# Optimization experiments

Hardware: AMD Instinct MI355X
Metric: run time of the kernel (lower is better)

Reference implementation:

```python
import jax, jax.numpy as jnp
import numpy as np

N = 100000      # nodes
E = 1600000     # edges
F_IN = 128      # input feature dim (x_s)
H = 64          # neuron
CF = 16         # attention_num_feature
G = 256         # graphs in batch


def setup_inputs() -> dict:
    key = jax.random.key(0)
    ks = jax.random.split(key, 20)
    w = lambda k, s: (jax.random.normal(k, s, jnp.float32) * 0.1)
    return {
        "x": jax.random.normal(ks[0], (N, F_IN), jnp.float32),
        "edge_index": jax.random.randint(ks[1], (2, E), 0, N, dtype=jnp.int64),
        "batch": jnp.sort(jax.random.randint(ks[2], (N,), 0, G, dtype=jnp.int64)),
        "closeness": jax.random.normal(ks[3], (N, CF), jnp.float32),
        "W1l": w(ks[4], (F_IN, H)), "b1l": jnp.zeros((H,), jnp.float32), "W1r": w(ks[5], (F_IN, H)),
        "W2l": w(ks[6], (H, H)),   "b2l": jnp.zeros((H,), jnp.float32), "W2r": w(ks[7], (H, H)),
        "W3l": w(ks[8], (H, H)),   "b3l": jnp.zeros((H,), jnp.float32), "W3r": w(ks[9], (H, H)),
        "Wc": w(ks[10], (CF, 1)),  "bc": jnp.zeros((1,), jnp.float32),
        "Wa1": w(ks[11], (H, 16)), "ba1": jnp.zeros((16,), jnp.float32),
        "Wa2": w(ks[12], (16, 1)), "ba2": jnp.zeros((1,), jnp.float32),
    }


def _sage_conv_max(x, src, dst, Wl, bl, Wr):
    # PyG SAGEConv(aggr='max'): lin_l(max_j x_j) + lin_r(x_i)
    msg = x[src]                                            # [E, F]
    agg = jax.ops.segment_max(msg, dst, num_segments=N)     # [N, F]
    agg = jnp.where(jnp.isfinite(agg), agg, 0.0)            # empty neighborhoods -> 0
    return agg @ Wl + bl + x @ Wr


def reference(x, edge_index, batch, closeness,
              W1l, b1l, W1r, W2l, b2l, W2r, W3l, b3l, W3r,
              Wc, bc, Wa1, ba1, Wa2, ba2):
    src, dst = edge_index[0], edge_index[1]
    h = jax.nn.relu(_sage_conv_max(x, src, dst, W1l, b1l, W1r))
    h = jax.nn.relu(_sage_conv_max(h, src, dst, W2l, b2l, W2r))
    h = jax.nn.relu(_sage_conv_max(h, src, dst, W3l, b3l, W3r))   # [N, H]

    # per-graph softmax attention (self_max aggregator), fused via segment ops
    c = closeness @ Wc + bc                                  # [N, 1]
    cmax = jax.ops.segment_max(c, batch, num_segments=G)     # [G, 1]
    e = jnp.exp(c - cmax[batch])                             # [N, 1]
    denom = jax.ops.segment_sum(e, batch, num_segments=G)    # [G, 1]
    p = e / denom[batch]                                     # softmax within each graph
    counts = jax.ops.segment_sum(jnp.ones((x.shape[0],), jnp.float32), batch, num_segments=G)
    p = p * counts[batch][:, None]                           # * curr_size

    pooled = jax.ops.segment_max(p * h, batch, num_segments=G)   # [G, H]
    pooled = jnp.where(jnp.isfinite(pooled), pooled, 0.0)
    a = jax.nn.relu(pooled @ Wa1 + ba1)
    return a @ Wa2 + ba2                                     # [G, 1]
```

## Files before the change

### kernel.cpp

```cpp
#include <hip/hip_runtime.h>
#include <math.h>

typedef unsigned int uint32;
typedef __attribute__((ext_vector_type(8))) short short8;
typedef __attribute__((ext_vector_type(4))) float f32x4;

#define BSH 7
#define NBMAX 800
#define CHUNK 4096


__device__ __forceinline__ unsigned fkey(float f) {
  unsigned u = __float_as_uint(f);
  return (u & 0x80000000u) ? ~u : (u | 0x80000000u);
}
__device__ __forceinline__ float funkey(unsigned k) {
  unsigned u = (k & 0x80000000u) ? (k ^ 0x80000000u) : ~k;
  return __uint_as_float(u);
}
__device__ __forceinline__ unsigned short f2bf(float f) {
  unsigned u = __float_as_uint(f);
  unsigned r = (u + 0x7FFFu + ((u >> 16) & 1u)) >> 16;
  return (unsigned short)r;
}
__device__ __forceinline__ float bf2f(unsigned short s) {
  return __uint_as_float(((unsigned)s) << 16);
}
__device__ __forceinline__ float blo(uint32 u) { return __uint_as_float(u << 16); }
__device__ __forceinline__ float bhi(uint32 u) { return __uint_as_float(u & 0xFFFF0000u); }
__device__ __forceinline__ uint32 cvtpk(float lo, float hi) {
  uint32 r;
  asm("v_cvt_pk_bf16_f32 %0, %1, %2" : "=v"(r) : "v"(lo), "v"(hi));
  return r;
}
__device__ __forceinline__ f32x4 mfma16(short8 a, short8 b, f32x4 c) {
  return __builtin_amdgcn_mfma_f32_16x16x32_bf16(a, b, c, 0, 0, 0);
}


__global__ void init_kernel(int* __restrict__ cnt, unsigned* __restrict__ pooledU,
                            unsigned* __restrict__ cmaxU, float* __restrict__ denom,
                            int* __restrict__ gcnt, int n, int gh, int g) {
  int i = blockIdx.x * blockDim.x + threadIdx.x;
  if (i < n) cnt[i] = 0;
  if (i < gh) pooledU[i] = 0x80000000u;
  if (i < g) { cmaxU[i] = 0u; denom[i] = 0.f; gcnt[i] = 0; }
}


__global__ void cvt_bf16_kernel(const float* __restrict__ in, unsigned short* __restrict__ out,
                                int n4) {
  int i = blockIdx.x * blockDim.x + threadIdx.x;
  if (i < n4) {
    float4 v = ((const float4*)in)[i];
    ushort4 o;
    o.x = f2bf(v.x);
    o.y = f2bf(v.y);
    o.z = f2bf(v.z);
    o.w = f2bf(v.w);
    ((ushort4*)out)[i] = o;
  }
}


__global__ void pack_bfrag_kernel(const float* __restrict__ W1l, const float* __restrict__ W1r,
                                  const float* __restrict__ W2l, const float* __restrict__ W2r,
                                  const float* __restrict__ W3l, const float* __restrict__ W3r,
                                  uint32* __restrict__ out) {
  int i = blockIdx.x * blockDim.x + threadIdx.x;
  if (i >= 32768) return;
  int set = i >> 14;
  int r = i & 16383;
  int g = r >> 8;
  int lane = (r >> 2) & 63;
  int p = r & 3;
  const float *Wl, *Wr;
  int F, nt, ks;
  if (g < 32) {
    F = 128; Wl = W1l; Wr = W1r; nt = g >> 3; ks = g & 7;
  } else if (g < 48) {
    F = 64; Wl = W2l; Wr = W2r; int q = g - 32; nt = q >> 2; ks = q & 3;
  } else {
    F = 64; Wl = W3l; Wr = W3r; int q = g - 48; nt = q >> 2; ks = q & 3;
  }
  int col = nt * 16 + (lane & 15);
  int k0 = ks * 32 + ((lane >> 4) << 3) + 2 * p;
  float w0 = (k0 < F) ? Wl[k0 * 64 + col] : Wr[(k0 - F) * 64 + col];
  int k1 = k0 + 1;
  float w1 = (k1 < F) ? Wl[k1 * 64 + col] : Wr[(k1 - F) * 64 + col];
  if (set) {
    w0 -= bf2f(f2bf(w0));
    w1 -= bf2f(f2bf(w1));
  }
  out[i] = ((uint32)f2bf(w1) << 16) | (uint32)f2bf(w0);
}


__global__ void hist_kernel(const int* __restrict__ dst, int* __restrict__ hist,
                            int E, int NB, int NC) {
  __shared__ int lcnt[NBMAX];
  int t = threadIdx.x, c = blockIdx.x;
  for (int i = t; i < NB; i += 256) lcnt[i] = 0;
  __syncthreads();
  int e0 = c * CHUNK, e1 = min(e0 + CHUNK, E);
  for (int e = e0 + t; e < e1; e += 256) atomicAdd(&lcnt[dst[e] >> BSH], 1);
  __syncthreads();
  for (int i = t; i < NB; i += 256) hist[(size_t)i * NC + c] = lcnt[i];
}

__global__ void rowscan_kernel(int* __restrict__ hist, int* __restrict__ bsum, int NB, int NC) {
  int wv = blockIdx.x * 4 + (threadIdx.x >> 6);
  int lane = threadIdx.x & 63;
  if (wv >= NB) return;
  int* row = hist + (size_t)wv * NC;
  int run = 0;
  for (int c = 0; c < NC; c += 64) {
    int idx = c + lane;
    int v = (idx < NC) ? row[idx] : 0;
    int incl = v;
#pragma unroll
    for (int off = 1; off < 64; off <<= 1) {
      int tt = __shfl_up(incl, off);
      if (lane >= off) incl += tt;
    }
    int tot = __shfl(incl, 63);
    if (idx < NC) row[idx] = run + incl - v;
    run += tot;
  }
  if (lane == 0) bsum[wv] = run;
}

__global__ void binscan_kernel(const int* __restrict__ bsum, int* __restrict__ bbase, int NB) {
  int lane = threadIdx.x;
  int run = 0;
  for (int c = 0; c < NB; c += 64) {
    int idx = c + lane;
    int v = (idx < NB) ? bsum[idx] : 0;
    int incl = v;
#pragma unroll
    for (int off = 1; off < 64; off <<= 1) {
      int tt = __shfl_up(incl, off);
      if (lane >= off) incl += tt;
    }
    if (idx < NB) bbase[idx] = run + incl - v;
    run += __shfl(incl, 63);
  }
  if (lane == 0) bbase[NB] = run;
}

__global__ void bfill_kernel(const int* __restrict__ src, const int* __restrict__ dst,
                             const int* __restrict__ hist, const int* __restrict__ bbase,
                             uint32* __restrict__ bbuf, int E, int NB, int NC) {
  __shared__ int lcur[NBMAX];
  int t = threadIdx.x, c = blockIdx.x;
  for (int i = t; i < NB; i += 256) lcur[i] = bbase[i] + hist[(size_t)i * NC + c];
  __syncthreads();
  int e0 = c * CHUNK, e1 = min(e0 + CHUNK, E);
  for (int e = e0 + t; e < e1; e += 256) {
    int d = dst[e], s = src[e];
    int b = d >> BSH;
    int pos = atomicAdd(&lcur[b], 1);
    bbuf[pos] = ((uint32)s << BSH) | (uint32)(d & ((1 << BSH) - 1));
  }
}

__global__ void place_kernel(const int* __restrict__ bbase, const uint32* __restrict__ bbuf,
                             int* __restrict__ cnt, int* __restrict__ csr, int N) {
  __shared__ int lcnt[1 << BSH];
  int b = blockIdx.x, t = threadIdx.x;
  for (int i = t; i < (1 << BSH); i += 256) lcnt[i] = 0;
  __syncthreads();
  int s0 = bbase[b], s1 = bbase[b + 1];
  for (int i = s0 + t; i < s1; i += 256) {
    uint32 rec = bbuf[i];
    int dl = rec & ((1 << BSH) - 1);
    int s = (int)(rec >> BSH);
    int pos = atomicAdd(&lcnt[dl], 1);
    if (pos < 64) csr[(((b << BSH) + dl) << 6) + pos] = s;
  }
  __syncthreads();
  int base = b << BSH;
  for (int i = t; i < (1 << BSH); i += 256) {
    int d = base + i;
    if (d < N) cnt[d] = min(lcnt[i], 64);
  }
}


template <int F, bool OUT_F32>
__global__ void __launch_bounds__(256, 2) sage_layer(
    const unsigned short* __restrict__ xg,
    const int* __restrict__ cnt, const int* __restrict__ csr,
    const short8* __restrict__ BfHi, const short8* __restrict__ BfLo, int loff,
    const float* __restrict__ bl, float* __restrict__ outf,
    unsigned short* __restrict__ outb, int nn) {
  constexpr int NPW = 8;
  constexpr int PAD = F + 4;
  constexpr int KS = F / 16;
  const int lane = threadIdx.x & 63;
  const int wid = threadIdx.x >> 6;
  const int c = lane & 31;
  const int h = lane >> 5;
  const int blk = blockIdx.x * 32;
  __shared__ uint32 Abuf[32][PAD];

  for (int j = 0; j < NPW; ++j) {
    int nl = wid * NPW + j;
    int n = blk + nl;
    if constexpr (F == 128) {
      float m0 = 0.f, m1 = 0.f, m2 = 0.f, m3 = 0.f;
      uint32 sv = 0u;
      if (n < nn) {
        sv = *(const uint32*)(xg + (size_t)n * F + 2 * lane);
        int dg = cnt[n];
        if (dg > 64) dg = 64;
        int k0 = n << 6, k1 = k0 + dg;
        if (k1 > k0) {
          m0 = -INFINITY; m1 = -INFINITY; m2 = -INFINITY; m3 = -INFINITY;
          int k = k0;
          for (; k + 8 <= k1; k += 8) {
            int i0 = csr[k + h], i1 = csr[k + 2 + h];
            int i2 = csr[k + 4 + h], i3 = csr[k + 6 + h];
            uint2 a = *(const uint2*)(xg + (size_t)i0 * F + 4 * c);
            uint2 b = *(const uint2*)(xg + (size_t)i1 * F + 4 * c);
            uint2 d = *(const uint2*)(xg + (size_t)i2 * F + 4 * c);
            uint2 e = *(const uint2*)(xg + (size_t)i3 * F + 4 * c);
            m0 = fmaxf(m0, fmaxf(fmaxf(blo(a.x), blo(b.x)), fmaxf(blo(d.x), blo(e.x))));
            m1 = fmaxf(m1, fmaxf(fmaxf(bhi(a.x), bhi(b.x)), fmaxf(bhi(d.x), bhi(e.x))));
            m2 = fmaxf(m2, fmaxf(fmaxf(blo(a.y), blo(b.y)), fmaxf(blo(d.y), blo(e.y))));
            m3 = fmaxf(m3, fmaxf(fmaxf(bhi(a.y), bhi(b.y)), fmaxf(bhi(d.y), bhi(e.y))));
          }
          for (; k + 2 <= k1; k += 2) {
            int i0 = csr[k + h];
            uint2 a = *(const uint2*)(xg + (size_t)i0 * F + 4 * c);
            m0 = fmaxf(m0, blo(a.x));
            m1 = fmaxf(m1, bhi(a.x));
            m2 = fmaxf(m2, blo(a.y));
            m3 = fmaxf(m3, bhi(a.y));
          }
          if (k < k1) {
            int i0 = csr[k];
            uint2 a = *(const uint2*)(xg + (size_t)i0 * F + 4 * c);
            m0 = fmaxf(m0, blo(a.x));
            m1 = fmaxf(m1, bhi(a.x));
            m2 = fmaxf(m2, blo(a.y));
            m3 = fmaxf(m3, bhi(a.y));
          }
          m0 = fmaxf(m0, __shfl_xor(m0, 32));
          m1 = fmaxf(m1, __shfl_xor(m1, 32));
          m2 = fmaxf(m2, __shfl_xor(m2, 32));
          m3 = fmaxf(m3, __shfl_xor(m3, 32));
        }
      }
      if (h == 0) {
        uint2 mm;
        mm.x = cvtpk(m0, m1);
        mm.y = cvtpk(m2, m3);
        *(uint2*)&Abuf[nl][2 * c] = mm;
      }
      Abuf[nl][64 + lane] = sv;
    } else {
      float m0 = 0.f, m1 = 0.f;
      uint32 sv = 0u;
      if (n < nn) {
        if (h == 0) sv = *(const uint32*)(xg + (size_t)n * F + 2 * c);
        int dg = cnt[n];
        if (dg > 64) dg = 64;
        int k0 = n << 6, k1 = k0 + dg;
        if (k1 > k0) {
          m0 = -INFINITY; m1 = -INFINITY;
          int k = k0;
          for (; k + 8 <= k1; k += 8) {
            int i0 = csr[k + h], i1 = csr[k + 2 + h];
            int i2 = csr[k + 4 + h], i3 = csr[k + 6 + h];
            uint32 a = *(const uint32*)(xg + (size_t)i0 * F + 2 * c);
            uint32 b = *(const uint32*)(xg + (size_t)i1 * F + 2 * c);
            uint32 d = *(const uint32*)(xg + (size_t)i2 * F + 2 * c);
            uint32 e = *(const uint32*)(xg + (size_t)i3 * F + 2 * c);
            m0 = fmaxf(m0, fmaxf(fmaxf(blo(a), blo(b)), fmaxf(blo(d), blo(e))));
            m1 = fmaxf(m1, fmaxf(fmaxf(bhi(a), bhi(b)), fmaxf(bhi(d), bhi(e))));
          }
          for (; k + 2 <= k1; k += 2) {
            int i0 = csr[k + h];
            uint32 a = *(const uint32*)(xg + (size_t)i0 * F + 2 * c);
            m0 = fmaxf(m0, blo(a));
            m1 = fmaxf(m1, bhi(a));
          }
          if (k < k1) {
            int i0 = csr[k];
            uint32 a = *(const uint32*)(xg + (size_t)i0 * F + 2 * c);
            m0 = fmaxf(m0, blo(a));
            m1 = fmaxf(m1, bhi(a));
          }
          m0 = fmaxf(m0, __shfl_xor(m0, 32));
          m1 = fmaxf(m1, __shfl_xor(m1, 32));
        }
      }
      if (h == 0) {
        Abuf[nl][c] = cvtpk(m0, m1);
        Abuf[nl][32 + c] = sv;
      }
    }
  }
  __syncthreads();

  const int l15 = lane & 15, lk = lane >> 4;
  const int mt = wid & 1;
  const int ntb = (wid >> 1) << 1;
  const int arow = mt * 16 + l15;
  float bb0 = bl[ntb * 16 + l15], bb1 = bl[ntb * 16 + 16 + l15];
  f32x4 acc0 = {bb0, bb0, bb0, bb0};
  f32x4 acc1 = {bb1, bb1, bb1, bb1};
  const int gb0 = (loff + (ntb + 0) * KS) * 64 + lane;
  const int gb1 = (loff + (ntb + 1) * KS) * 64 + lane;
#pragma unroll 2
  for (int ks = 0; ks < KS; ++ks) {
    short8 a = *(const short8*)&Abuf[arow][ks * 16 + lk * 4];
    short8 bh0 = BfHi[gb0 + ks * 64];
    short8 bl0 = BfLo[gb0 + ks * 64];
    short8 bh1 = BfHi[gb1 + ks * 64];
    short8 bl1 = BfLo[gb1 + ks * 64];
    acc0 = mfma16(a, bh0, acc0);
    acc0 = mfma16(a, bl0, acc0);
    acc1 = mfma16(a, bh1, acc1);
    acc1 = mfma16(a, bl1, acc1);
  }
#pragma unroll
  for (int j = 0; j < 4; ++j) {
    int node = blk + mt * 16 + lk * 4 + j;
    if (node < nn) {
      float r0 = fmaxf(acc0[j], 0.f);
      float r1 = fmaxf(acc1[j], 0.f);
      if constexpr (OUT_F32) {
        outf[(size_t)node * 64 + ntb * 16 + l15] = r0;
        outf[(size_t)node * 64 + ntb * 16 + 16 + l15] = r1;
      } else {
        outb[(size_t)node * 64 + ntb * 16 + l15] = f2bf(r0);
        outb[(size_t)node * 64 + ntb * 16 + 16 + l15] = f2bf(r1);
      }
    }
  }
}


__global__ void cscore_kernel(const float* __restrict__ clo, const float* __restrict__ Wc,
                              const float* __restrict__ bc, const int* __restrict__ bat,
                              float* __restrict__ cbuf, unsigned* __restrict__ cmaxU,
                              int* __restrict__ gcnt, int n) {
  int i = blockIdx.x * blockDim.x + threadIdx.x;
  int lane = threadIdx.x & 63;
  float cv = -INFINITY;
  int g = -1;
  if (i < n) {
    const float4* row = (const float4*)(clo + (size_t)i * 16);
    float4 r0 = row[0], r1 = row[1], r2 = row[2], r3 = row[3];
    cv = bc[0];
    cv += r0.x * Wc[0] + r0.y * Wc[1] + r0.z * Wc[2] + r0.w * Wc[3];
    cv += r1.x * Wc[4] + r1.y * Wc[5] + r1.z * Wc[6] + r1.w * Wc[7];
    cv += r2.x * Wc[8] + r2.y * Wc[9] + r2.z * Wc[10] + r2.w * Wc[11];
    cv += r3.x * Wc[12] + r3.y * Wc[13] + r3.z * Wc[14] + r3.w * Wc[15];
    cbuf[i] = cv;
    g = bat[i];
  }
  int g0 = __shfl(g, 0), g63 = __shfl(g, 63);
  if (g0 >= 0 && g0 == g63) {
    float m = cv;
#pragma unroll
    for (int off = 32; off; off >>= 1) m = fmaxf(m, __shfl_down(m, off));
    if (lane == 0) {
      atomicMax(&cmaxU[g0], fkey(m));
      atomicAdd(&gcnt[g0], 64);
    }
  } else if (g >= 0) {
    atomicMax(&cmaxU[g], fkey(cv));
    atomicAdd(&gcnt[g], 1);
  }
}

__global__ void esum_kernel(const float* __restrict__ cbuf, const int* __restrict__ bat,
                            const unsigned* __restrict__ cmaxU, float* __restrict__ ebuf,
                            float* __restrict__ denom, int n) {
  int i = blockIdx.x * blockDim.x + threadIdx.x;
  int lane = threadIdx.x & 63;
  float ev = 0.f;
  int g = -1;
  if (i < n) {
    g = bat[i];
    float cm = funkey(cmaxU[g]);
    ev = expf(cbuf[i] - cm);
    ebuf[i] = ev;
  }
  int g0 = __shfl(g, 0), g63 = __shfl(g, 63);
  if (g0 >= 0 && g0 == g63) {
    float s = ev;
#pragma unroll
    for (int off = 32; off; off >>= 1) s += __shfl_down(s, off);
    if (lane == 0) atomicAdd(&denom[g0], s);
  } else if (g >= 0) {
    atomicAdd(&denom[g], ev);
  }
}

__global__ void pool_kernel(const float* __restrict__ ebuf, const float* __restrict__ denom,
                            const int* __restrict__ gcnt, const int* __restrict__ bat,
                            const float* __restrict__ h3, unsigned* __restrict__ pooledU,
                            int n) {
  const int CH = 64;
  int wave = (blockIdx.x * blockDim.x + threadIdx.x) >> 6;
  int lane = threadIdx.x & 63;
  int nb = wave * CH;
  if (nb >= n) return;
  int ne = min(nb + CH, n);
  int curg = bat[nb];
  float factor = (float)gcnt[curg] / denom[curg];
  float lmax = -INFINITY;
  for (int nd = nb; nd < ne; ++nd) {
    int g = bat[nd];
    if (g != curg) {
      atomicMax(&pooledU[(size_t)curg * 64 + lane], fkey(lmax));
      curg = g;
      factor = (float)gcnt[g] / denom[g];
      lmax = -INFINITY;
    }
    float v = ebuf[nd] * factor * h3[(size_t)nd * 64 + lane];
    lmax = fmaxf(lmax, v);
  }
  atomicMax(&pooledU[(size_t)curg * 64 + lane], fkey(lmax));
}

__global__ void final_kernel(const unsigned* __restrict__ pooledU, const float* __restrict__ Wa1,
                             const float* __restrict__ ba1, const float* __restrict__ Wa2,
                             const float* __restrict__ ba2, float* __restrict__ out, int G) {
  int g = blockIdx.x;
  int lane = threadIdx.x;
  float v = funkey(pooledU[(size_t)g * 64 + lane]);
  if (!isfinite(v)) v = 0.f;
  float outv = 0.f;
#pragma unroll
  for (int j = 0; j < 16; ++j) {
    float psum = v * Wa1[lane * 16 + j];
#pragma unroll
    for (int off = 32; off; off >>= 1) psum += __shfl_down(psum, off);
    if (lane == 0) outv += fmaxf(psum + ba1[j], 0.f) * Wa2[j];
  }
  if (lane == 0) out[g] = outv + ba2[0];
}


static inline size_t alignup(size_t x) { return (x + 255) & ~(size_t)255; }

extern "C" void kernel_launch(void* const* d_in, const int* in_sizes, int n_in,
                              void* d_out, int out_size, void* d_ws, size_t ws_size,
                              hipStream_t stream) {
  const float* x = (const float*)d_in[0];
  const int* ei = (const int*)d_in[1];
  const int* bat = (const int*)d_in[2];
  const float* clo = (const float*)d_in[3];
  const float* W1l = (const float*)d_in[4];
  const float* b1l = (const float*)d_in[5];
  const float* W1r = (const float*)d_in[6];
  const float* W2l = (const float*)d_in[7];
  const float* b2l = (const float*)d_in[8];
  const float* W2r = (const float*)d_in[9];
  const float* W3l = (const float*)d_in[10];
  const float* b3l = (const float*)d_in[11];
  const float* W3r = (const float*)d_in[12];
  const float* Wc = (const float*)d_in[13];
  const float* bc = (const float*)d_in[14];
  const float* Wa1 = (const float*)d_in[15];
  const float* ba1 = (const float*)d_in[16];
  const float* Wa2 = (const float*)d_in[17];
  const float* ba2 = (const float*)d_in[18];
  float* out = (float*)d_out;

  const int N = in_sizes[2];
  const int E = in_sizes[1] / 2;
  const int G = out_size;
  const int FIN = in_sizes[0] / N;

  char* p = (char*)d_ws;
  auto carve = [&](size_t bytes) {
    char* r = p;
    p += alignup(bytes);
    return r;
  };
  const int NB = (N + (1 << BSH) - 1) >> BSH;
  const int NC = (E + CHUNK - 1) / CHUNK;
  int* cnt = (int*)carve((size_t)N * 4);
  int* csr = (int*)carve((size_t)N * 64 * 4);
  unsigned short* xb = (unsigned short*)carve((size_t)N * FIN * 2);
  unsigned short* hb1 = (unsigned short*)carve((size_t)N * 64 * 2);
  unsigned short* hb2 = (unsigned short*)carve((size_t)N * 64 * 2);
  float* cbuf = (float*)carve((size_t)N * 4);
  float* ebuf = (float*)carve((size_t)N * 4);
  unsigned* cmaxU = (unsigned*)carve((size_t)G * 4);
  float* denom = (float*)carve((size_t)G * 4);
  int* gcnt = (int*)carve((size_t)G * 4);
  unsigned* pooledU = (unsigned*)carve((size_t)G * 64 * 4);
  uint32* Bfrag = (uint32*)carve((size_t)32768 * 4);
  int* hist = (int*)carve((size_t)NB * NC * 4);
  int* bsum = (int*)carve((size_t)NB * 4);
  int* bbase = (int*)carve((size_t)(NB + 1) * 4);
  uint32* bbuf = (uint32*)carve((size_t)E * 4);
  float* h3 = (float*)xb;

  const short8* BfHi = (const short8*)Bfrag;
  const short8* BfLo = (const short8*)(Bfrag + 16384);

  const int* srcv = ei;
  const int* dstv = ei + E;

  int nb = (N + 255) / 256;
  hipLaunchKernelGGL(init_kernel, dim3(nb), dim3(256), 0, stream, cnt, pooledU, cmaxU, denom,
                     gcnt, N, G * 64, G);
  int ncvt = (N * FIN) / 4;
  hipLaunchKernelGGL(cvt_bf16_kernel, dim3((ncvt + 255) / 256), dim3(256), 0, stream, x, xb,
                     ncvt);
  hipLaunchKernelGGL(pack_bfrag_kernel, dim3(128), dim3(256), 0, stream, W1l, W1r, W2l, W2r,
                     W3l, W3r, Bfrag);
  hipLaunchKernelGGL(hist_kernel, dim3(NC), dim3(256), 0, stream, dstv, hist, E, NB, NC);
  hipLaunchKernelGGL(rowscan_kernel, dim3((NB + 3) / 4), dim3(256), 0, stream, hist, bsum, NB,
                     NC);
  hipLaunchKernelGGL(binscan_kernel, dim3(1), dim3(64), 0, stream, bsum, bbase, NB);
  hipLaunchKernelGGL(bfill_kernel, dim3(NC), dim3(256), 0, stream, srcv, dstv, hist, bbase,
                     bbuf, E, NB, NC);
  hipLaunchKernelGGL(place_kernel, dim3(NB), dim3(256), 0, stream, bbase, bbuf, cnt, csr, N);

  int nblocks32 = (N + 31) / 32;
  hipLaunchKernelGGL((sage_layer<128, false>), dim3(nblocks32), dim3(256), 0, stream, xb, cnt,
                     csr, BfHi, BfLo, 0, b1l, (float*)nullptr, hb1, N);
  hipLaunchKernelGGL((sage_layer<64, false>), dim3(nblocks32), dim3(256), 0, stream, hb1, cnt,
                     csr, BfHi, BfLo, 32, b2l, (float*)nullptr, hb2, N);
  hipLaunchKernelGGL((sage_layer<64, true>), dim3(nblocks32), dim3(256), 0, stream, hb2, cnt,
                     csr, BfHi, BfLo, 48, b3l, h3, (unsigned short*)nullptr, N);

  hipLaunchKernelGGL(cscore_kernel, dim3(nb), dim3(256), 0, stream, clo, Wc, bc, bat, cbuf,
                     cmaxU, gcnt, N);
  hipLaunchKernelGGL(esum_kernel, dim3(nb), dim3(256), 0, stream, cbuf, bat, cmaxU, ebuf, denom,
                     N);
  int pw = (N + 63) / 64;
  int pb = (pw + 3) / 4;
  hipLaunchKernelGGL(pool_kernel, dim3(pb), dim3(256), 0, stream, ebuf, denom, gcnt, bat, h3,
                     pooledU, N);
  hipLaunchKernelGGL(final_kernel, dim3(G), dim3(64), 0, stream, pooledU, Wa1, ba1, Wa2, ba2,
                     out, G);
}
```

Measured before the change: 491.3 us.

## Use order-preserving bf16 keys with packed u16 max for neighbor aggregation

Layer 1 input is stored as order-preserving 16-bit keys, so the neighbor max becomes v_pk_max_u16 on packed pairs with no unpacking to fp32, and results are un-keyed once per node. Layers 2 and 3 take non-negative post-ReLU bf16 values, whose raw bit patterns already order correctly, so they use the same packed unsigned max. The gather loop is unrolled to 16 edges per step for more loads in flight. The cnt zeroing is also dropped from init, which assumes place_kernel writes every cnt entry; negative zero in layers 2-3 and the empty-neighborhood zero both depend on these orderings holding.

```diff
diff --git a/kernel.cpp b/kernel.cpp
--- a/kernel.cpp
+++ b/kernel.cpp
@@ -26,38 +26,40 @@
 __device__ __forceinline__ float bf2f(unsigned short s) {
   return __uint_as_float(((unsigned)s) << 16);
 }
-__device__ __forceinline__ float blo(uint32 u) { return __uint_as_float(u << 16); }
-__device__ __forceinline__ float bhi(uint32 u) { return __uint_as_float(u & 0xFFFF0000u); }
-__device__ __forceinline__ uint32 cvtpk(float lo, float hi) {
-  uint32 r;
-  asm("v_cvt_pk_bf16_f32 %0, %1, %2" : "=v"(r) : "v"(lo), "v"(hi));
-  return r;
+__device__ __forceinline__ uint32 pkmaxu(uint32 a, uint32 b) {
+  uint32 d;
+  asm("v_pk_max_u16 %0, %1, %2" : "=v"(d) : "v"(a), "v"(b));
+  return d;
+}
+__device__ __forceinline__ uint32 unkey2(uint32 m) {
+  uint32 t = (m >> 15) & 0x00010001u;
+  uint32 mask = (t * 0x7FFFu) ^ 0xFFFFFFFFu;
+  return m ^ mask;
 }
 __device__ __forceinline__ f32x4 mfma16(short8 a, short8 b, f32x4 c) {
   return __builtin_amdgcn_mfma_f32_16x16x32_bf16(a, b, c, 0, 0, 0);
 }
 
 
-__global__ void init_kernel(int* __restrict__ cnt, unsigned* __restrict__ pooledU,
-                            unsigned* __restrict__ cmaxU, float* __restrict__ denom,
-                            int* __restrict__ gcnt, int n, int gh, int g) {
+__global__ void init_kernel(unsigned* __restrict__ pooledU, unsigned* __restrict__ cmaxU,
+                            float* __restrict__ denom, int* __restrict__ gcnt, int gh, int g) {
   int i = blockIdx.x * blockDim.x + threadIdx.x;
-  if (i < n) cnt[i] = 0;
   if (i < gh) pooledU[i] = 0x80000000u;
   if (i < g) { cmaxU[i] = 0u; denom[i] = 0.f; gcnt[i] = 0; }
 }
 
 
-__global__ void cvt_bf16_kernel(const float* __restrict__ in, unsigned short* __restrict__ out,
-                                int n4) {
+__global__ void cvt_key_kernel(const float* __restrict__ in, unsigned short* __restrict__ out,
+                               int n4) {
   int i = blockIdx.x * blockDim.x + threadIdx.x;
   if (i < n4) {
     float4 v = ((const float4*)in)[i];
     ushort4 o;
-    o.x = f2bf(v.x);
-    o.y = f2bf(v.y);
-    o.z = f2bf(v.z);
-    o.w = f2bf(v.w);
+    unsigned short b;
+    b = f2bf(v.x); o.x = (b & 0x8000u) ? (unsigned short)~b : (unsigned short)(b | 0x8000u);
+    b = f2bf(v.y); o.y = (b & 0x8000u) ? (unsigned short)~b : (unsigned short)(b | 0x8000u);
+    b = f2bf(v.z); o.z = (b & 0x8000u) ? (unsigned short)~b : (unsigned short)(b | 0x8000u);
+    b = f2bf(v.w); o.w = (b & 0x8000u) ? (unsigned short)~b : (unsigned short)(b | 0x8000u);
     ((ushort4*)out)[i] = o;
   }
 }
@@ -197,6 +199,7 @@
   constexpr int NPW = 8;
   constexpr int PAD = F + 4;
   constexpr int KS = F / 16;
+  constexpr bool KEYED = (F == 128);
   const int lane = threadIdx.x & 63;
   const int wid = threadIdx.x >> 6;
   const int c = lane & 31;
@@ -208,96 +211,82 @@
     int nl = wid * NPW + j;
     int n = blk + nl;
     if constexpr (F == 128) {
-      float m0 = 0.f, m1 = 0.f, m2 = 0.f, m3 = 0.f;
-      uint32 sv = 0u;
+      uint32 m01 = 0u, m23 = 0u, sv = 0u;
       if (n < nn) {
-        sv = *(const uint32*)(xg + (size_t)n * F + 2 * lane);
+        sv = *(const uint32*)(xg + ((size_t)n << 7) + 2 * lane);
         int dg = cnt[n];
         if (dg > 64) dg = 64;
         int k0 = n << 6, k1 = k0 + dg;
         if (k1 > k0) {
-          m0 = -INFINITY; m1 = -INFINITY; m2 = -INFINITY; m3 = -INFINITY;
           int k = k0;
-          for (; k + 8 <= k1; k += 8) {
-            int i0 = csr[k + h], i1 = csr[k + 2 + h];
-            int i2 = csr[k + 4 + h], i3 = csr[k + 6 + h];
-            uint2 a = *(const uint2*)(xg + (size_t)i0 * F + 4 * c);
-            uint2 b = *(const uint2*)(xg + (size_t)i1 * F + 4 * c);
-            uint2 d = *(const uint2*)(xg + (size_t)i2 * F + 4 * c);
-            uint2 e = *(const uint2*)(xg + (size_t)i3 * F + 4 * c);
-            m0 = fmaxf(m0, fmaxf(fmaxf(blo(a.x), blo(b.x)), fmaxf(blo(d.x), blo(e.x))));
-            m1 = fmaxf(m1, fmaxf(fmaxf(bhi(a.x), bhi(b.x)), fmaxf(bhi(d.x), bhi(e.x))));
-            m2 = fmaxf(m2, fmaxf(fmaxf(blo(a.y), blo(b.y)), fmaxf(blo(d.y), blo(e.y))));
-            m3 = fmaxf(m3, fmaxf(fmaxf(bhi(a.y), bhi(b.y)), fmaxf(bhi(d.y), bhi(e.y))));
+#define LD128(i) (*(const uint2*)(xg + ((size_t)(i) << 7) + 4 * c))
+          for (; k + 16 <= k1; k += 16) {
+            int i0 = csr[k + h], i1 = csr[k + 2 + h], i2 = csr[k + 4 + h], i3 = csr[k + 6 + h];
+            int i4 = csr[k + 8 + h], i5 = csr[k + 10 + h], i6 = csr[k + 12 + h],
+                i7 = csr[k + 14 + h];
+            uint2 a0 = LD128(i0), a1 = LD128(i1), a2 = LD128(i2), a3 = LD128(i3);
+            uint2 a4 = LD128(i4), a5 = LD128(i5), a6 = LD128(i6), a7 = LD128(i7);
+            uint32 x0 = pkmaxu(pkmaxu(a0.x, a1.x), pkmaxu(a2.x, a3.x));
+            uint32 x1 = pkmaxu(pkmaxu(a4.x, a5.x), pkmaxu(a6.x, a7.x));
+            m01 = pkmaxu(m01, pkmaxu(x0, x1));
+            uint32 y0 = pkmaxu(pkmaxu(a0.y, a1.y), pkmaxu(a2.y, a3.y));
+            uint32 y1 = pkmaxu(pkmaxu(a4.y, a5.y), pkmaxu(a6.y, a7.y));
+            m23 = pkmaxu(m23, pkmaxu(y0, y1));
           }
           for (; k + 2 <= k1; k += 2) {
-            int i0 = csr[k + h];
-            uint2 a = *(const uint2*)(xg + (size_t)i0 * F + 4 * c);
-            m0 = fmaxf(m0, blo(a.x));
-            m1 = fmaxf(m1, bhi(a.x));
-            m2 = fmaxf(m2, blo(a.y));
-            m3 = fmaxf(m3, bhi(a.y));
+            uint2 a = LD128(csr[k + h]);
+            m01 = pkmaxu(m01, a.x);
+            m23 = pkmaxu(m23, a.y);
           }
           if (k < k1) {
-            int i0 = csr[k];
-            uint2 a = *(const uint2*)(xg + (size_t)i0 * F + 4 * c);
-            m0 = fmaxf(m0, blo(a.x));
-            m1 = fmaxf(m1, bhi(a.x));
-            m2 = fmaxf(m2, blo(a.y));
-            m3 = fmaxf(m3, bhi(a.y));
+            uint2 a = LD128(csr[k]);
+            m01 = pkmaxu(m01, a.x);
+            m23 = pkmaxu(m23, a.y);
           }
-          m0 = fmaxf(m0, __shfl_xor(m0, 32));
-          m1 = fmaxf(m1, __shfl_xor(m1, 32));
-          m2 = fmaxf(m2, __shfl_xor(m2, 32));
-          m3 = fmaxf(m3, __shfl_xor(m3, 32));
+#undef LD128
+          m01 = pkmaxu(m01, (uint32)__shfl_xor((int)m01, 32));
+          m23 = pkmaxu(m23, (uint32)__shfl_xor((int)m23, 32));
+          if constexpr (KEYED) {
+            m01 = unkey2(m01);
+            m23 = unkey2(m23);
+          }
         }
       }
       if (h == 0) {
         uint2 mm;
-        mm.x = cvtpk(m0, m1);
-        mm.y = cvtpk(m2, m3);
+        mm.x = m01;
+        mm.y = m23;
         *(uint2*)&Abuf[nl][2 * c] = mm;
       }
-      Abuf[nl][64 + lane] = sv;
+      Abuf[nl][64 + lane] = KEYED ? unkey2(sv) : sv;
     } else {
-      float m0 = 0.f, m1 = 0.f;
-      uint32 sv = 0u;
+      uint32 m01 = 0u, sv = 0u;
       if (n < nn) {
-        if (h == 0) sv = *(const uint32*)(xg + (size_t)n * F + 2 * c);
+        if (h == 0) sv = *(const uint32*)(xg + ((size_t)n << 6) + 2 * c);
         int dg = cnt[n];
         if (dg > 64) dg = 64;
         int k0 = n << 6, k1 = k0 + dg;
         if (k1 > k0) {
-          m0 = -INFINITY; m1 = -INFINITY;
           int k = k0;
-          for (; k + 8 <= k1; k += 8) {
-            int i0 = csr[k + h], i1 = csr[k + 2 + h];
-            int i2 = csr[k + 4 + h], i3 = csr[k + 6 + h];
-            uint32 a = *(const uint32*)(xg + (size_t)i0 * F + 2 * c);
-            uint32 b = *(const uint32*)(xg + (size_t)i1 * F + 2 * c);
-            uint32 d = *(const uint32*)(xg + (size_t)i2 * F + 2 * c);
-            uint32 e = *(const uint32*)(xg + (size_t)i3 * F + 2 * c);
-            m0 = fmaxf(m0, fmaxf(fmaxf(blo(a), blo(b)), fmaxf(blo(d), blo(e))));
-            m1 = fmaxf(m1, fmaxf(fmaxf(bhi(a), bhi(b)), fmaxf(bhi(d), bhi(e))));
+#define LD64(i) (*(const uint32*)(xg + ((size_t)(i) << 6) + 2 * c))
+          for (; k + 16 <= k1; k += 16) {
+            int i0 = csr[k + h], i1 = csr[k + 2 + h], i2 = csr[k + 4 + h], i3 = csr[k + 6 + h];
+            int i4 = csr[k + 8 + h], i5 = csr[k + 10 + h], i6 = csr[k + 12 + h],
+                i7 = csr[k + 14 + h];
+            uint32 a0 = LD64(i0), a1 = LD64(i1), a2 = LD64(i2), a3 = LD64(i3);
+            uint32 a4 = LD64(i4), a5 = LD64(i5), a6 = LD64(i6), a7 = LD64(i7);
+            uint32 x0 = pkmaxu(pkmaxu(a0, a1), pkmaxu(a2, a3));
+            uint32 x1 = pkmaxu(pkmaxu(a4, a5), pkmaxu(a6, a7));
+            m01 = pkmaxu(m01, pkmaxu(x0, x1));
           }
-          for (; k + 2 <= k1; k += 2) {
-            int i0 = csr[k + h];
-            uint32 a = *(const uint32*)(xg + (size_t)i0 * F + 2 * c);
-            m0 = fmaxf(m0, blo(a));
-            m1 = fmaxf(m1, bhi(a));
-          }
-          if (k < k1) {
-            int i0 = csr[k];
-            uint32 a = *(const uint32*)(xg + (size_t)i0 * F + 2 * c);
-            m0 = fmaxf(m0, blo(a));
-            m1 = fmaxf(m1, bhi(a));
-          }
-          m0 = fmaxf(m0, __shfl_xor(m0, 32));
-          m1 = fmaxf(m1, __shfl_xor(m1, 32));
+          for (; k + 2 <= k1; k += 2) m01 = pkmaxu(m01, LD64(csr[k + h]));
+          if (k < k1) m01 = pkmaxu(m01, LD64(csr[k]));
+#undef LD64
+          m01 = pkmaxu(m01, (uint32)__shfl_xor((int)m01, 32));
         }
       }
       if (h == 0) {
-        Abuf[nl][c] = cvtpk(m0, m1);
+        Abuf[nl][c] = m01;
         Abuf[nl][32 + c] = sv;
       }
     }
@@ -511,10 +500,10 @@
   const int* dstv = ei + E;
 
   int nb = (N + 255) / 256;
-  hipLaunchKernelGGL(init_kernel, dim3(nb), dim3(256), 0, stream, cnt, pooledU, cmaxU, denom,
-                     gcnt, N, G * 64, G);
+  hipLaunchKernelGGL(init_kernel, dim3((G * 64 + 255) / 256), dim3(256), 0, stream, pooledU,
+                     cmaxU, denom, gcnt, G * 64, G);
   int ncvt = (N * FIN) / 4;
-  hipLaunchKernelGGL(cvt_bf16_kernel, dim3((ncvt + 255) / 256), dim3(256), 0, stream, x, xb,
+  hipLaunchKernelGGL(cvt_key_kernel, dim3((ncvt + 255) / 256), dim3(256), 0, stream, x, xb,
                      ncvt);
   hipLaunchKernelGGL(pack_bfrag_kernel, dim3(128), dim3(256), 0, stream, W1l, W1r, W2l, W2r,
                      W3l, W3r, Bfrag);
```

Measured after the change: 521.0 us. 1.06x slower.
